# Performance work log

Measured on AMD Instinct MI355X. Metric: run time of the kernel, lower is better.

Reference implementation:

```python
import jax, jax.numpy as jnp
import numpy as np

N = 256   # n_nodes == input_dim (table columns)
B = 1024  # batch size
D = 64    # decoder_dim / encoder_dim


def setup_inputs() -> dict:
    key = jax.random.key(0)
    ks = jax.random.split(key, 10)
    r = lambda k, sh, s=0.05: jax.random.normal(k, sh, dtype=jnp.float32) * s
    return {
        "x": jax.random.normal(ks[0], (B, N), dtype=jnp.float32),
        "eps": jax.random.normal(ks[1], (B, N), dtype=jnp.float32),
        "graph_logits": r(ks[2], (N, N), 0.5),
        "W_enc": r(ks[3], (N, D)),
        "b_enc": jnp.zeros((D,), jnp.float32),
        "W_mu": r(ks[4], (D, N)),
        "b_mu": jnp.zeros((N,), jnp.float32),
        "W_lv": r(ks[5], (D, N)),
        "b_lv": jnp.zeros((N,), jnp.float32),
        "emb_W": r(ks[6], (N, N + 1, D)),   # per-column Linear(input_dim+1 -> decoder_dim)
        "emb_b": jnp.zeros((N, D), jnp.float32),
        "gc1_W": r(ks[7], (D, D // 2)),
        "gc1_b": jnp.zeros((D // 2,), jnp.float32),
        "gc2_W": r(ks[8], (D // 2, 1)),
        "gc2_b": jnp.zeros((1,), jnp.float32),
        "it_num": 10,
    }


def _graph_conv(h, adj, W, b):
    # DGL GraphConv(norm='both', weight, bias) with edge_weight = adj values.
    # Edges go row->col of adj; degrees are unweighted nonzero counts.
    dt = h.dtype
    deg_out = jnp.sum(adj != 0, axis=1).astype(dt)  # out-degree of source node
    deg_in = jnp.sum(adj != 0, axis=0).astype(dt)   # in-degree of destination node
    norm_src = deg_out ** -0.5
    norm_dst = deg_in ** -0.5
    h = h * norm_src[None, :, None]                 # scale source features
    agg = jnp.einsum('bnd,nm->bmd', h, adj)         # sum_i adj[i,j] * h[:, i]
    agg = agg * norm_dst[None, :, None]
    return agg @ W + b


def reference(x, eps, graph_logits, W_enc, b_enc, W_mu, b_mu, W_lv, b_lv,
              emb_W, emb_b, gc1_W, gc1_b, gc2_W, gc2_b, it_num):
    # --- Encoder (MLP-VAE, encoder_l=2 => single Linear+ReLU trunk) ---
    h = jax.nn.relu(x @ W_enc + b_enc)
    mu = h @ W_mu + b_mu
    logvar = h @ W_lv + b_lv
    z = mu + eps * jnp.exp(0.5 * logvar)            # reparameterize, (B, N)
    # --- LearnedGraph ---
    g = jax.nn.sigmoid(graph_logits)
    eye = jnp.eye(N, dtype=g.dtype)
    adj = g * (1.0 - eye) + eye                      # force self-loops to 1
    if it_num > 50:                                  # nn.Threshold(threshold, 0)
        adj = jnp.where(adj > 0.1, adj, 0.0)
    # --- GraphInputProcessorHomo: het encoding + per-column embeddings ---
    b_z = jnp.concatenate(
        [z[:, :, None], jnp.broadcast_to(eye, (z.shape[0], N, N))], axis=-1
    )                                                # (B, N, N+1)
    b_z = jnp.tanh(jnp.einsum('bnf,nfd->bnd', b_z, emb_W) + emb_b[None])  # (B, N, D)
    # --- GraphDecoderHomo ('gcn'): GraphConv(64->32, tanh) -> GraphConv(32->1) ---
    h1 = jnp.tanh(_graph_conv(b_z, adj, gc1_W, gc1_b))
    h2 = _graph_conv(h1, adj, gc2_W, gc2_b)          # (B, N, 1)
    x_hat = h2.reshape(z.shape[0], -1)               # (B, N)
    return x_hat
```

## Files before the change

kernel.cpp:

```cpp
#include <hip/hip_runtime.h>
#include <hip/hip_bf16.h>
#include <math.h>

#define NN 256
#define BB 1024
#define DD 64

typedef short bf16x8 __attribute__((ext_vector_type(8)));
typedef float f32x4 __attribute__((ext_vector_type(4)));

__device__ __forceinline__ float ftanh(float x) {
    float e = __expf(2.0f * x);
    return 1.0f - 2.0f * __builtin_amdgcn_rcpf(e + 1.0f);
}

__device__ __forceinline__ unsigned short f2bf(float v) {
    __hip_bfloat16 h = __float2bfloat16(v);
    return *reinterpret_cast<unsigned short*>(&h);
}

__device__ __forceinline__ float bf2f(unsigned short u) {
    union { unsigned int i; float f; } c;
    c.i = ((unsigned int)u) << 16;
    return c.f;
}

__global__ __launch_bounds__(256) void k12(
    const float* __restrict__ x, const float* __restrict__ Wenc,
    const float* __restrict__ benc, const float* __restrict__ Wmu,
    const float* __restrict__ bmu, const float* __restrict__ Wlv,
    const float* __restrict__ blv, const float* __restrict__ eps,
    float* __restrict__ ZT)
{
    __shared__ float Hs[4][DD];
    int t = threadIdx.x;
    int b0 = blockIdx.x << 2;
    {
        int d = t & 63, bl = t >> 6;
        const float* xr = x + (b0 + bl) * NN;
        float acc = benc[d];
        for (int n = 0; n < NN; n += 4) {
            float4 xv = *(const float4*)&xr[n];
            acc = fmaf(xv.x, Wenc[(n + 0) * DD + d], acc);
            acc = fmaf(xv.y, Wenc[(n + 1) * DD + d], acc);
            acc = fmaf(xv.z, Wenc[(n + 2) * DD + d], acc);
            acc = fmaf(xv.w, Wenc[(n + 3) * DD + d], acc);
        }
        Hs[bl][d] = fmaxf(acc, 0.0f);
    }
    __syncthreads();
    {
        int n = t;
        float mu[4], lv[4];
        float bm = bmu[n], bl_ = blv[n];
#pragma unroll
        for (int i = 0; i < 4; ++i) { mu[i] = bm; lv[i] = bl_; }
        for (int d = 0; d < DD; ++d) {
            float wm = Wmu[d * NN + n];
            float wl = Wlv[d * NN + n];
#pragma unroll
            for (int i = 0; i < 4; ++i) {
                float h = Hs[i][d];
                mu[i] = fmaf(h, wm, mu[i]);
                lv[i] = fmaf(h, wl, lv[i]);
            }
        }
#pragma unroll
        for (int i = 0; i < 4; ++i) {
            int b = b0 + i;
            ZT[n * BB + b] = fmaf(eps[b * NN + n], expf(0.5f * lv[i]), mu[i]);
        }
    }
}

__global__ __launch_bounds__(256) void k3a(
    const float* __restrict__ gl, const int* __restrict__ itp,
    float* __restrict__ adj, float* __restrict__ dego)
{
    int nrow = blockIdx.x, m = threadIdx.x;
    float v = gl[nrow * NN + m];
    float a = (nrow == m) ? 1.0f : 1.0f / (1.0f + expf(-v));
    if (itp[0] > 50 && !(a > 0.1f)) a = 0.0f;
    adj[nrow * NN + m] = a;
    unsigned long long ball = __ballot(a != 0.0f);
    __shared__ int cnt_s[4];
    if ((m & 63) == 0) cnt_s[m >> 6] = __popcll(ball);
    __syncthreads();
    if (m == 0) dego[nrow] = (float)(cnt_s[0] + cnt_s[1] + cnt_s[2] + cnt_s[3]);
}

__global__ __launch_bounds__(256) void k3b(
    const float* __restrict__ adj, const float* __restrict__ dego,
    float* __restrict__ adjw, unsigned short* __restrict__ adjwt)
{
    int m = blockIdx.x, nrow = threadIdx.x;
    float a = adj[nrow * NN + m];
    unsigned long long ball = __ballot(a != 0.0f);
    __shared__ int cnt_s[4];
    __shared__ float din_s;
    if ((nrow & 63) == 0) cnt_s[nrow >> 6] = __popcll(ball);
    __syncthreads();
    if (nrow == 0) din_s = (float)(cnt_s[0] + cnt_s[1] + cnt_s[2] + cnt_s[3]);
    __syncthreads();
    float w = a * (1.0f / sqrtf(dego[nrow])) * (1.0f / sqrtf(din_s));
    adjw[nrow * NN + m] = w;
    adjwt[m * NN + nrow] = f2bf(w);
}

__global__ __launch_bounds__(256) void k4_mfma(
    const float* __restrict__ ZT, const float* __restrict__ embW,
    const float* __restrict__ embB, const float* __restrict__ g1W,
    unsigned short* __restrict__ P1TT)
{
    __shared__ float As[4][64], Cs[4][64], zs[4][64];
    __shared__ float Ws[32][68];
    __shared__ __align__(16) unsigned short Dst[64][32][4];
    int t = threadIdx.x;
    int w = t >> 6, l = t & 63;
    int lo = l & 15, q = l >> 4;
    int q8 = q << 3;
    int nb = blockIdx.x & 63, bb = blockIdx.x >> 6;
    int n0 = nb << 2, b0 = bb << 6;

    {
        int ni = t >> 6, d = t & 63;
        size_t eb = (size_t)(n0 + ni) * (257 * 64);
        As[ni][d] = embW[eb + d];
        Cs[ni][d] = embW[eb + ((size_t)(n0 + ni + 1) << 6) + d]
                  + embB[((n0 + ni) << 6) + d];
        zs[ni][d] = ZT[(size_t)(n0 + ni) * BB + b0 + d];
    }
    for (int i = t; i < 2048; i += 256) {
        int d = i >> 5, k = i & 31;
        Ws[k][d] = g1W[i];
    }
    __syncthreads();

    bf16x8 bwh[2][2], bwl[2][2];
#pragma unroll
    for (int nt = 0; nt < 2; ++nt)
#pragma unroll
        for (int kc = 0; kc < 2; ++kc) {
            float4 w0 = *(const float4*)&Ws[(nt << 4) + lo][(kc << 5) + q8];
            float4 w1 = *(const float4*)&Ws[(nt << 4) + lo][(kc << 5) + q8 + 4];
            float v[8] = {w0.x, w0.y, w0.z, w0.w, w1.x, w1.y, w1.z, w1.w};
            bf16x8 h, lq;
#pragma unroll
            for (int j = 0; j < 8; ++j) {
                unsigned short hb = f2bf(v[j]);
                h[j] = (short)hb;
                lq[j] = (short)f2bf(v[j] - bf2f(hb));
            }
            bwh[nt][kc] = h;
            bwl[nt][kc] = lq;
        }

#pragma unroll
    for (int ni = 0; ni < 4; ++ni) {
        float zv = zs[ni][(w << 4) + lo];
        f32x4 acc0 = (f32x4)0.0f, acc1 = (f32x4)0.0f;
#pragma unroll
        for (int kc = 0; kc < 2; ++kc) {
            float4 a0 = *(const float4*)&As[ni][(kc << 5) + q8];
            float4 a1 = *(const float4*)&As[ni][(kc << 5) + q8 + 4];
            float4 c0 = *(const float4*)&Cs[ni][(kc << 5) + q8];
            float4 c1 = *(const float4*)&Cs[ni][(kc << 5) + q8 + 4];
            float e[8];
            e[0] = ftanh(fmaf(zv, a0.x, c0.x));
            e[1] = ftanh(fmaf(zv, a0.y, c0.y));
            e[2] = ftanh(fmaf(zv, a0.z, c0.z));
            e[3] = ftanh(fmaf(zv, a0.w, c0.w));
            e[4] = ftanh(fmaf(zv, a1.x, c1.x));
            e[5] = ftanh(fmaf(zv, a1.y, c1.y));
            e[6] = ftanh(fmaf(zv, a1.z, c1.z));
            e[7] = ftanh(fmaf(zv, a1.w, c1.w));
            bf16x8 ehi, elo;
#pragma unroll
            for (int j = 0; j < 8; ++j) {
                unsigned short hb = f2bf(e[j]);
                ehi[j] = (short)hb;
                elo[j] = (short)f2bf(e[j] - bf2f(hb));
            }
            acc0 = __builtin_amdgcn_mfma_f32_16x16x32_bf16(ehi, bwh[0][kc], acc0, 0, 0, 0);
            acc0 = __builtin_amdgcn_mfma_f32_16x16x32_bf16(elo, bwh[0][kc], acc0, 0, 0, 0);
            acc0 = __builtin_amdgcn_mfma_f32_16x16x32_bf16(ehi, bwl[0][kc], acc0, 0, 0, 0);
            acc1 = __builtin_amdgcn_mfma_f32_16x16x32_bf16(ehi, bwh[1][kc], acc1, 0, 0, 0);
            acc1 = __builtin_amdgcn_mfma_f32_16x16x32_bf16(elo, bwh[1][kc], acc1, 0, 0, 0);
            acc1 = __builtin_amdgcn_mfma_f32_16x16x32_bf16(ehi, bwl[1][kc], acc1, 0, 0, 0);
        }
        int bl = (w << 4) + (q << 2);
#pragma unroll
        for (int r = 0; r < 4; ++r) {
            Dst[bl + r][lo][ni]      = f2bf(acc0[r]);
            Dst[bl + r][16 + lo][ni] = f2bf(acc1[r]);
        }
    }
    __syncthreads();

    const uint2* dsp = (const uint2*)&Dst[0][0][0];
    size_t obase = ((size_t)b0 * 32) * NN + n0;
#pragma unroll
    for (int i = 0; i < 8; ++i) {
        int p = (i << 8) + t;
        uint2 v = dsp[p];
        *(uint2*)&P1TT[obase + (size_t)p * NN] = v;
    }
}

__global__ __launch_bounds__(256) void k5_mfma(
    const unsigned short* __restrict__ adjwt, const unsigned short* __restrict__ p1tt,
    const float* __restrict__ g1b, const float* __restrict__ g2w,
    float* __restrict__ Q)
{
    int t = threadIdx.x;
    int w = t >> 6, l = t & 63;
    int c = l & 15, q = l >> 4;
    int jt = blockIdx.x >> 1, mh = blockIdx.x & 1;
    int j0 = jt << 6;
    int mbase = (mh << 7) + (w << 5);

    f32x4 acc[2][4];
#pragma unroll
    for (int i = 0; i < 2; ++i)
#pragma unroll
        for (int j = 0; j < 4; ++j) acc[i][j] = (f32x4)0.0f;

    const unsigned short* ap[2];
    const unsigned short* bp[4];
#pragma unroll
    for (int mi = 0; mi < 2; ++mi)
        ap[mi] = adjwt + (size_t)(mbase + (mi << 4) + c) * NN + (q << 3);
#pragma unroll
    for (int ji = 0; ji < 4; ++ji)
        bp[ji] = p1tt + (size_t)(j0 + (ji << 4) + c) * NN + (q << 3);

#pragma unroll 2
    for (int n0 = 0; n0 < NN; n0 += 32) {
        bf16x8 af[2], bf[4];
#pragma unroll
        for (int mi = 0; mi < 2; ++mi) af[mi] = *(const bf16x8*)(ap[mi] + n0);
#pragma unroll
        for (int ji = 0; ji < 4; ++ji) bf[ji] = *(const bf16x8*)(bp[ji] + n0);
#pragma unroll
        for (int mi = 0; mi < 2; ++mi)
#pragma unroll
            for (int ji = 0; ji < 4; ++ji)
                acc[mi][ji] = __builtin_amdgcn_mfma_f32_16x16x32_bf16(
                    af[mi], bf[ji], acc[mi][ji], 0, 0, 0);
    }

    float b1v0 = g1b[c],      g2v0 = g2w[c];
    float b1v1 = g1b[16 + c], g2v1 = g2w[16 + c];
    int bb0 = jt << 1;
#pragma unroll
    for (int mi = 0; mi < 2; ++mi) {
#pragma unroll
        for (int bb = 0; bb < 2; ++bb) {
            float red[4];
#pragma unroll
            for (int r = 0; r < 4; ++r) {
                float s = ftanh(acc[mi][(bb << 1) + 0][r] + b1v0) * g2v0
                        + ftanh(acc[mi][(bb << 1) + 1][r] + b1v1) * g2v1;
                s += __shfl_xor(s, 1);
                s += __shfl_xor(s, 2);
                s += __shfl_xor(s, 4);
                s += __shfl_xor(s, 8);
                red[r] = s;
            }
            float* qp = &Q[(size_t)(bb0 + bb) * NN + mbase + (mi << 4) + (q << 2)];
            if (c == 0) qp[0] = red[0];
            if (c == 1) qp[1] = red[1];
            if (c == 2) qp[2] = red[2];
            if (c == 3) qp[3] = red[3];
        }
    }
}

__global__ __launch_bounds__(256) void k6_gc2(
    const float* __restrict__ Q, const float* __restrict__ adjw,
    const float* __restrict__ g2b, float* __restrict__ xh)
{
    __shared__ float At[32][33];
    __shared__ float Bt[32][33];
    int t = threadIdx.x;
    int tx = t & 15, ty = t >> 4;
    int mt = blockIdx.x & 7, bt = blockIdx.x >> 3;
    int m0 = mt << 5, b0 = bt << 5;
    float acc[2][2] = {{0.0f, 0.0f}, {0.0f, 0.0f}};

    for (int kb = 0; kb < NN; kb += 32) {
        for (int i = t; i < 1024; i += 256) {
            int r = i >> 5, cc = i & 31;
            At[r][cc] = Q[(b0 + r) * NN + kb + cc];
            Bt[r][cc] = adjw[(kb + r) * NN + m0 + cc];
        }
        __syncthreads();
#pragma unroll 8
        for (int kk = 0; kk < 32; ++kk) {
            float bv0 = Bt[kk][tx << 1], bv1 = Bt[kk][(tx << 1) + 1];
            float a0 = At[ty << 1][kk], a1 = At[(ty << 1) + 1][kk];
            acc[0][0] = fmaf(a0, bv0, acc[0][0]);
            acc[0][1] = fmaf(a0, bv1, acc[0][1]);
            acc[1][0] = fmaf(a1, bv0, acc[1][0]);
            acc[1][1] = fmaf(a1, bv1, acc[1][1]);
        }
        __syncthreads();
    }
    float bias = g2b[0];
#pragma unroll
    for (int i = 0; i < 2; ++i) {
        float2 v = make_float2(acc[i][0] + bias, acc[i][1] + bias);
        *(float2*)&xh[(b0 + (ty << 1) + i) * NN + m0 + (tx << 1)] = v;
    }
}

extern "C" void kernel_launch(void* const* d_in, const int* in_sizes, int n_in,
                              void* d_out, int out_size, void* d_ws, size_t ws_size,
                              hipStream_t stream) {
    const float* x    = (const float*)d_in[0];
    const float* eps  = (const float*)d_in[1];
    const float* gl   = (const float*)d_in[2];
    const float* Wenc = (const float*)d_in[3];
    const float* benc = (const float*)d_in[4];
    const float* Wmu  = (const float*)d_in[5];
    const float* bmu  = (const float*)d_in[6];
    const float* Wlv  = (const float*)d_in[7];
    const float* blv  = (const float*)d_in[8];
    const float* embW = (const float*)d_in[9];
    const float* embB = (const float*)d_in[10];
    const float* g1W  = (const float*)d_in[11];
    const float* g1b  = (const float*)d_in[12];
    const float* g2W  = (const float*)d_in[13];
    const float* g2b  = (const float*)d_in[14];
    const int*   itp  = (const int*)d_in[15];

    float* ws   = (float*)d_ws;
    float* ZT   = ws + 65536;
    float* ADJR = ws + 327680;
    float* DEGO = ws + 393216;
    float* ADJW = ws + 393472;
    unsigned short* ADJWT = (unsigned short*)(ws + 459008);
    unsigned short* P1TT  = (unsigned short*)(ws + 491776);
    float* Qb   = ws + 4686080;
    float* xh   = (float*)d_out;

    k12     <<<256,  256, 0, stream>>>(x, Wenc, benc, Wmu, bmu, Wlv, blv, eps, ZT);
    k3a     <<<256,  256, 0, stream>>>(gl, itp, ADJR, DEGO);
    k3b     <<<256,  256, 0, stream>>>(ADJR, DEGO, ADJW, ADJWT);
    k4_mfma <<<1024, 256, 0, stream>>>(ZT, embW, embB, g1W, P1TT);
    k5_mfma <<<1024, 256, 0, stream>>>(ADJWT, P1TT, g1b, g2W, Qb);
    k6_gc2  <<<256,  256, 0, stream>>>(Qb, ADJW, g2b, xh);
}
```

Measured before the change: 180.5 us.

## Merge independent stages into shared launches to cut kernel count

The encoder kernel and the adjacency-sigmoid kernel become one launch whose blocks branch on block index. The adjacency normalisation is folded into the embedding/GC1 kernel, whose blocks now each process two tiles instead of one, halving that grid to 512 blocks. This removes two launches and lets the bf16 weight split be amortised over two tiles per block. The cost is branchy blocks and some blocks doing extra adjacency work before their MFMA tiles, which may cause imbalance.

```diff
diff --git a/kernel.cpp b/kernel.cpp
--- a/kernel.cpp
+++ b/kernel.cpp
@@ -25,189 +25,199 @@
     return c.f;
 }
 
-__global__ __launch_bounds__(256) void k12(
-    const float* __restrict__ x, const float* __restrict__ Wenc,
+__global__ __launch_bounds__(256) void kA(
+    const float* __restrict__ x, const float* __restrict__ eps,
+    const float* __restrict__ gl, const float* __restrict__ Wenc,
     const float* __restrict__ benc, const float* __restrict__ Wmu,
     const float* __restrict__ bmu, const float* __restrict__ Wlv,
-    const float* __restrict__ blv, const float* __restrict__ eps,
-    float* __restrict__ ZT)
+    const float* __restrict__ blv, const int* __restrict__ itp,
+    float* __restrict__ ZT, float* __restrict__ ADJ, float* __restrict__ DEGO)
 {
     __shared__ float Hs[4][DD];
+    __shared__ int cnt_s[4];
     int t = threadIdx.x;
-    int b0 = blockIdx.x << 2;
-    {
-        int d = t & 63, bl = t >> 6;
-        const float* xr = x + (b0 + bl) * NN;
-        float acc = benc[d];
-        for (int n = 0; n < NN; n += 4) {
-            float4 xv = *(const float4*)&xr[n];
-            acc = fmaf(xv.x, Wenc[(n + 0) * DD + d], acc);
-            acc = fmaf(xv.y, Wenc[(n + 1) * DD + d], acc);
-            acc = fmaf(xv.z, Wenc[(n + 2) * DD + d], acc);
-            acc = fmaf(xv.w, Wenc[(n + 3) * DD + d], acc);
-        }
-        Hs[bl][d] = fmaxf(acc, 0.0f);
-    }
-    __syncthreads();
-    {
-        int n = t;
-        float mu[4], lv[4];
-        float bm = bmu[n], bl_ = blv[n];
-#pragma unroll
-        for (int i = 0; i < 4; ++i) { mu[i] = bm; lv[i] = bl_; }
-        for (int d = 0; d < DD; ++d) {
-            float wm = Wmu[d * NN + n];
-            float wl = Wlv[d * NN + n];
+    int bid = blockIdx.x;
+
+    if (bid < 256) {
+        int b0 = bid << 2;
+        {
+            int d = t & 63, bl = t >> 6;
+            const float* xr = x + (b0 + bl) * NN;
+            float acc = benc[d];
+            for (int n = 0; n < NN; n += 4) {
+                float4 xv = *(const float4*)&xr[n];
+                acc = fmaf(xv.x, Wenc[(n + 0) * DD + d], acc);
+                acc = fmaf(xv.y, Wenc[(n + 1) * DD + d], acc);
+                acc = fmaf(xv.z, Wenc[(n + 2) * DD + d], acc);
+                acc = fmaf(xv.w, Wenc[(n + 3) * DD + d], acc);
+            }
+            Hs[bl][d] = fmaxf(acc, 0.0f);
+        }
+        __syncthreads();
+        {
+            int n = t;
+            float mu[4], lv[4];
+            float bm = bmu[n], bl_ = blv[n];
+#pragma unroll
+            for (int i = 0; i < 4; ++i) { mu[i] = bm; lv[i] = bl_; }
+            for (int d = 0; d < DD; ++d) {
+                float wm = Wmu[d * NN + n];
+                float wl = Wlv[d * NN + n];
+#pragma unroll
+                for (int i = 0; i < 4; ++i) {
+                    float h = Hs[i][d];
+                    mu[i] = fmaf(h, wm, mu[i]);
+                    lv[i] = fmaf(h, wl, lv[i]);
+                }
+            }
 #pragma unroll
             for (int i = 0; i < 4; ++i) {
-                float h = Hs[i][d];
-                mu[i] = fmaf(h, wm, mu[i]);
-                lv[i] = fmaf(h, wl, lv[i]);
-            }
-        }
-#pragma unroll
-        for (int i = 0; i < 4; ++i) {
-            int b = b0 + i;
-            ZT[n * BB + b] = fmaf(eps[b * NN + n], expf(0.5f * lv[i]), mu[i]);
-        }
-    }
-}
-
-__global__ __launch_bounds__(256) void k3a(
-    const float* __restrict__ gl, const int* __restrict__ itp,
-    float* __restrict__ adj, float* __restrict__ dego)
-{
-    int nrow = blockIdx.x, m = threadIdx.x;
-    float v = gl[nrow * NN + m];
-    float a = (nrow == m) ? 1.0f : 1.0f / (1.0f + expf(-v));
-    if (itp[0] > 50 && !(a > 0.1f)) a = 0.0f;
-    adj[nrow * NN + m] = a;
-    unsigned long long ball = __ballot(a != 0.0f);
-    __shared__ int cnt_s[4];
-    if ((m & 63) == 0) cnt_s[m >> 6] = __popcll(ball);
-    __syncthreads();
-    if (m == 0) dego[nrow] = (float)(cnt_s[0] + cnt_s[1] + cnt_s[2] + cnt_s[3]);
-}
-
-__global__ __launch_bounds__(256) void k3b(
-    const float* __restrict__ adj, const float* __restrict__ dego,
-    float* __restrict__ adjw, unsigned short* __restrict__ adjwt)
-{
-    int m = blockIdx.x, nrow = threadIdx.x;
-    float a = adj[nrow * NN + m];
-    unsigned long long ball = __ballot(a != 0.0f);
-    __shared__ int cnt_s[4];
-    __shared__ float din_s;
-    if ((nrow & 63) == 0) cnt_s[nrow >> 6] = __popcll(ball);
-    __syncthreads();
-    if (nrow == 0) din_s = (float)(cnt_s[0] + cnt_s[1] + cnt_s[2] + cnt_s[3]);
-    __syncthreads();
-    float w = a * (1.0f / sqrtf(dego[nrow])) * (1.0f / sqrtf(din_s));
-    adjw[nrow * NN + m] = w;
-    adjwt[m * NN + nrow] = f2bf(w);
-}
-
-__global__ __launch_bounds__(256) void k4_mfma(
+                int b = b0 + i;
+                ZT[n * BB + b] = fmaf(eps[b * NN + n], expf(0.5f * lv[i]), mu[i]);
+            }
+        }
+    } else {
+        int nrow = bid - 256, m = t;
+        float v = gl[nrow * NN + m];
+        float a = (nrow == m) ? 1.0f : 1.0f / (1.0f + expf(-v));
+        if (itp[0] > 50 && !(a > 0.1f)) a = 0.0f;
+        ADJ[nrow * NN + m] = a;
+        unsigned long long ball = __ballot(a != 0.0f);
+        if ((m & 63) == 0) cnt_s[m >> 6] = __popcll(ball);
+        __syncthreads();
+        if (m == 0) DEGO[nrow] = (float)(cnt_s[0] + cnt_s[1] + cnt_s[2] + cnt_s[3]);
+    }
+}
+
+__global__ __launch_bounds__(256) void kB(
     const float* __restrict__ ZT, const float* __restrict__ embW,
     const float* __restrict__ embB, const float* __restrict__ g1W,
+    const float* __restrict__ ADJ, const float* __restrict__ DEGO,
+    float* __restrict__ ADJW, unsigned short* __restrict__ ADJWT,
     unsigned short* __restrict__ P1TT)
 {
-    __shared__ float As[4][64], Cs[4][64], zs[4][64];
-    __shared__ float Ws[32][68];
-    __shared__ __align__(16) unsigned short Dst[64][32][4];
+    __shared__ __align__(16) unsigned char smem[28160];
     int t = threadIdx.x;
-    int w = t >> 6, l = t & 63;
-    int lo = l & 15, q = l >> 4;
-    int q8 = q << 3;
-    int nb = blockIdx.x & 63, bb = blockIdx.x >> 6;
-    int n0 = nb << 2, b0 = bb << 6;
+    int bid = blockIdx.x;
+
+    if (bid < 256) {
+        int m = bid;
+        int* cnt_s = (int*)smem;
+        float* din_s = (float*)(smem + 16);
+        float a = ADJ[t * NN + m];
+        unsigned long long ball = __ballot(a != 0.0f);
+        if ((t & 63) == 0) cnt_s[t >> 6] = __popcll(ball);
+        __syncthreads();
+        if (t == 0) din_s[0] = (float)(cnt_s[0] + cnt_s[1] + cnt_s[2] + cnt_s[3]);
+        __syncthreads();
+        float wv = a * (1.0f / sqrtf(DEGO[t])) * (1.0f / sqrtf(din_s[0]));
+        ADJW[t * NN + m] = wv;
+        ADJWT[m * NN + t] = f2bf(wv);
+    }
 
     {
-        int ni = t >> 6, d = t & 63;
-        size_t eb = (size_t)(n0 + ni) * (257 * 64);
-        As[ni][d] = embW[eb + d];
-        Cs[ni][d] = embW[eb + ((size_t)(n0 + ni + 1) << 6) + d]
-                  + embB[((n0 + ni) << 6) + d];
-        zs[ni][d] = ZT[(size_t)(n0 + ni) * BB + b0 + d];
-    }
-    for (int i = t; i < 2048; i += 256) {
-        int d = i >> 5, k = i & 31;
-        Ws[k][d] = g1W[i];
-    }
-    __syncthreads();
-
-    bf16x8 bwh[2][2], bwl[2][2];
-#pragma unroll
-    for (int nt = 0; nt < 2; ++nt)
-#pragma unroll
-        for (int kc = 0; kc < 2; ++kc) {
-            float4 w0 = *(const float4*)&Ws[(nt << 4) + lo][(kc << 5) + q8];
-            float4 w1 = *(const float4*)&Ws[(nt << 4) + lo][(kc << 5) + q8 + 4];
-            float v[8] = {w0.x, w0.y, w0.z, w0.w, w1.x, w1.y, w1.z, w1.w};
-            bf16x8 h, lq;
-#pragma unroll
-            for (int j = 0; j < 8; ++j) {
-                unsigned short hb = f2bf(v[j]);
-                h[j] = (short)hb;
-                lq[j] = (short)f2bf(v[j] - bf2f(hb));
-            }
-            bwh[nt][kc] = h;
-            bwl[nt][kc] = lq;
-        }
-
-#pragma unroll
-    for (int ni = 0; ni < 4; ++ni) {
-        float zv = zs[ni][(w << 4) + lo];
-        f32x4 acc0 = (f32x4)0.0f, acc1 = (f32x4)0.0f;
-#pragma unroll
-        for (int kc = 0; kc < 2; ++kc) {
-            float4 a0 = *(const float4*)&As[ni][(kc << 5) + q8];
-            float4 a1 = *(const float4*)&As[ni][(kc << 5) + q8 + 4];
-            float4 c0 = *(const float4*)&Cs[ni][(kc << 5) + q8];
-            float4 c1 = *(const float4*)&Cs[ni][(kc << 5) + q8 + 4];
-            float e[8];
-            e[0] = ftanh(fmaf(zv, a0.x, c0.x));
-            e[1] = ftanh(fmaf(zv, a0.y, c0.y));
-            e[2] = ftanh(fmaf(zv, a0.z, c0.z));
-            e[3] = ftanh(fmaf(zv, a0.w, c0.w));
-            e[4] = ftanh(fmaf(zv, a1.x, c1.x));
-            e[5] = ftanh(fmaf(zv, a1.y, c1.y));
-            e[6] = ftanh(fmaf(zv, a1.z, c1.z));
-            e[7] = ftanh(fmaf(zv, a1.w, c1.w));
-            bf16x8 ehi, elo;
-#pragma unroll
-            for (int j = 0; j < 8; ++j) {
-                unsigned short hb = f2bf(e[j]);
-                ehi[j] = (short)hb;
-                elo[j] = (short)f2bf(e[j] - bf2f(hb));
-            }
-            acc0 = __builtin_amdgcn_mfma_f32_16x16x32_bf16(ehi, bwh[0][kc], acc0, 0, 0, 0);
-            acc0 = __builtin_amdgcn_mfma_f32_16x16x32_bf16(elo, bwh[0][kc], acc0, 0, 0, 0);
-            acc0 = __builtin_amdgcn_mfma_f32_16x16x32_bf16(ehi, bwl[0][kc], acc0, 0, 0, 0);
-            acc1 = __builtin_amdgcn_mfma_f32_16x16x32_bf16(ehi, bwh[1][kc], acc1, 0, 0, 0);
-            acc1 = __builtin_amdgcn_mfma_f32_16x16x32_bf16(elo, bwh[1][kc], acc1, 0, 0, 0);
-            acc1 = __builtin_amdgcn_mfma_f32_16x16x32_bf16(ehi, bwl[1][kc], acc1, 0, 0, 0);
-        }
-        int bl = (w << 4) + (q << 2);
-#pragma unroll
-        for (int r = 0; r < 4; ++r) {
-            Dst[bl + r][lo][ni]      = f2bf(acc0[r]);
-            Dst[bl + r][16 + lo][ni] = f2bf(acc1[r]);
-        }
-    }
-    __syncthreads();
-
-    const uint2* dsp = (const uint2*)&Dst[0][0][0];
-    size_t obase = ((size_t)b0 * 32) * NN + n0;
-#pragma unroll
-    for (int i = 0; i < 8; ++i) {
-        int p = (i << 8) + t;
-        uint2 v = dsp[p];
-        *(uint2*)&P1TT[obase + (size_t)p * NN] = v;
-    }
-}
-
-__global__ __launch_bounds__(256) void k5_mfma(
+        float (*As)[64] = (float(*)[64])(smem);
+        float (*Cs)[64] = (float(*)[64])(smem + 1024);
+        float (*zsm)[64] = (float(*)[64])(smem + 2048);
+        float (*Ws)[68] = (float(*)[68])(smem + 3072);
+        unsigned short (*Dst)[32][4] = (unsigned short(*)[32][4])(smem + 11776);
+        int w = t >> 6, l = t & 63;
+        int lo = l & 15, q = l >> 4;
+        int q8 = q << 3;
+
+        for (int i = t; i < 2048; i += 256) {
+            int d = i >> 5, k = i & 31;
+            Ws[k][d] = g1W[i];
+        }
+        __syncthreads();
+
+        bf16x8 bwh[2][2], bwl[2][2];
+#pragma unroll
+        for (int nt = 0; nt < 2; ++nt)
+#pragma unroll
+            for (int kc = 0; kc < 2; ++kc) {
+                float4 w0 = *(const float4*)&Ws[(nt << 4) + lo][(kc << 5) + q8];
+                float4 w1 = *(const float4*)&Ws[(nt << 4) + lo][(kc << 5) + q8 + 4];
+                float v[8] = {w0.x, w0.y, w0.z, w0.w, w1.x, w1.y, w1.z, w1.w};
+                bf16x8 h, lq;
+#pragma unroll
+                for (int j = 0; j < 8; ++j) {
+                    unsigned short hb = f2bf(v[j]);
+                    h[j] = (short)hb;
+                    lq[j] = (short)f2bf(v[j] - bf2f(hb));
+                }
+                bwh[nt][kc] = h;
+                bwl[nt][kc] = lq;
+            }
+
+        for (int it = 0; it < 2; ++it) {
+            int tile = (bid << 1) | it;
+            int nb = tile & 63, bb2 = tile >> 6;
+            int n0 = nb << 2, b0 = bb2 << 6;
+            __syncthreads();
+            {
+                int ni = t >> 6, d = t & 63;
+                size_t eb = (size_t)(n0 + ni) * (257 * 64);
+                As[ni][d] = embW[eb + d];
+                Cs[ni][d] = embW[eb + ((size_t)(n0 + ni + 1) << 6) + d]
+                          + embB[((n0 + ni) << 6) + d];
+                zsm[ni][d] = ZT[(size_t)(n0 + ni) * BB + b0 + d];
+            }
+            __syncthreads();
+#pragma unroll
+            for (int ni = 0; ni < 4; ++ni) {
+                float zv = zsm[ni][(w << 4) + lo];
+                f32x4 acc0 = (f32x4)0.0f, acc1 = (f32x4)0.0f;
+#pragma unroll
+                for (int kc = 0; kc < 2; ++kc) {
+                    float4 a0 = *(const float4*)&As[ni][(kc << 5) + q8];
+                    float4 a1 = *(const float4*)&As[ni][(kc << 5) + q8 + 4];
+                    float4 c0 = *(const float4*)&Cs[ni][(kc << 5) + q8];
+                    float4 c1 = *(const float4*)&Cs[ni][(kc << 5) + q8 + 4];
+                    float e[8];
+                    e[0] = ftanh(fmaf(zv, a0.x, c0.x));
+                    e[1] = ftanh(fmaf(zv, a0.y, c0.y));
+                    e[2] = ftanh(fmaf(zv, a0.z, c0.z));
+                    e[3] = ftanh(fmaf(zv, a0.w, c0.w));
+                    e[4] = ftanh(fmaf(zv, a1.x, c1.x));
+                    e[5] = ftanh(fmaf(zv, a1.y, c1.y));
+                    e[6] = ftanh(fmaf(zv, a1.z, c1.z));
+                    e[7] = ftanh(fmaf(zv, a1.w, c1.w));
+                    bf16x8 ehi, elo;
+#pragma unroll
+                    for (int j = 0; j < 8; ++j) {
+                        unsigned short hb = f2bf(e[j]);
+                        ehi[j] = (short)hb;
+                        elo[j] = (short)f2bf(e[j] - bf2f(hb));
+                    }
+                    acc0 = __builtin_amdgcn_mfma_f32_16x16x32_bf16(ehi, bwh[0][kc], acc0, 0, 0, 0);
+                    acc0 = __builtin_amdgcn_mfma_f32_16x16x32_bf16(elo, bwh[0][kc], acc0, 0, 0, 0);
+                    acc0 = __builtin_amdgcn_mfma_f32_16x16x32_bf16(ehi, bwl[0][kc], acc0, 0, 0, 0);
+                    acc1 = __builtin_amdgcn_mfma_f32_16x16x32_bf16(ehi, bwh[1][kc], acc1, 0, 0, 0);
+                    acc1 = __builtin_amdgcn_mfma_f32_16x16x32_bf16(elo, bwh[1][kc], acc1, 0, 0, 0);
+                    acc1 = __builtin_amdgcn_mfma_f32_16x16x32_bf16(ehi, bwl[1][kc], acc1, 0, 0, 0);
+                }
+                int bl = (w << 4) + (q << 2);
+#pragma unroll
+                for (int r = 0; r < 4; ++r) {
+                    Dst[bl + r][lo][ni]      = f2bf(acc0[r]);
+                    Dst[bl + r][16 + lo][ni] = f2bf(acc1[r]);
+                }
+            }
+            __syncthreads();
+            const uint2* dsp = (const uint2*)&Dst[0][0][0];
+            size_t obase = ((size_t)b0 * 32) * NN + n0;
+#pragma unroll
+            for (int i = 0; i < 8; ++i) {
+                int p = (i << 8) + t;
+                uint2 v = dsp[p];
+                *(uint2*)&P1TT[obase + (size_t)p * NN] = v;
+            }
+        }
+    }
+}
+
+__global__ __launch_bounds__(256) void kC(
     const unsigned short* __restrict__ adjwt, const unsigned short* __restrict__ p1tt,
     const float* __restrict__ g1b, const float* __restrict__ g2w,
     float* __restrict__ Q)
@@ -276,7 +286,7 @@
     }
 }
 
-__global__ __launch_bounds__(256) void k6_gc2(
+__global__ __launch_bounds__(256) void kD(
     const float* __restrict__ Q, const float* __restrict__ adjw,
     const float* __restrict__ g2b, float* __restrict__ xh)
 {
@@ -336,7 +346,7 @@
 
     float* ws   = (float*)d_ws;
     float* ZT   = ws + 65536;
-    float* ADJR = ws + 327680;
+    float* ADJ  = ws + 327680;
     float* DEGO = ws + 393216;
     float* ADJW = ws + 393472;
     unsigned short* ADJWT = (unsigned short*)(ws + 459008);
@@ -344,10 +354,9 @@
     float* Qb   = ws + 4686080;
     float* xh   = (float*)d_out;
 
-    k12     <<<256,  256, 0, stream>>>(x, Wenc, benc, Wmu, bmu, Wlv, blv, eps, ZT);
-    k3a     <<<256,  256, 0, stream>>>(gl, itp, ADJR, DEGO);
-    k3b     <<<256,  256, 0, stream>>>(ADJR, DEGO, ADJW, ADJWT);
-    k4_mfma <<<1024, 256, 0, stream>>>(ZT, embW, embB, g1W, P1TT);
-    k5_mfma <<<1024, 256, 0, stream>>>(ADJWT, P1TT, g1b, g2W, Qb);
-    k6_gc2  <<<256,  256, 0, stream>>>(Qb, ADJW, g2b, xh);
-}
+    kA<<<512,  256, 0, stream>>>(x, eps, gl, Wenc, benc, Wmu, bmu, Wlv, blv,
+                                 itp, ZT, ADJ, DEGO);
+    kB<<<512,  256, 0, stream>>>(ZT, embW, embB, g1W, ADJ, DEGO, ADJW, ADJWT, P1TT);
+    kC<<<1024, 256, 0, stream>>>(ADJWT, P1TT, g1b, g2W, Qb);
+    kD<<<256,  256, 0, stream>>>(Qb, ADJW, g2b, xh);
+}
```

Measured after the change: 178.4 us. Within noise of the previous version (-1.2%).
